# Kernel optimization log

Hardware: AMD Instinct MI355X
Metric: run time of the kernel (lower is better)

## Reference

```python
import math
import jax, jax.numpy as jnp
import numpy as np

DIM, HEADS, HD = 384, 12, 32
FEAT, WIN, SHIFT = (64, 64), (8, 8), (4, 4)
L = WIN[0] * WIN[1]  # window area = 64
MAX_LOGIT = math.log(1.0 / 0.01)


def _rel_log_coords():
    # pair-wise relative positions, log-spaced (static, numpy)
    coords = np.stack(np.meshgrid(np.arange(WIN[0]), np.arange(WIN[1]), indexing='ij'), 0).reshape(2, -1)
    rel = (coords[:, :, None] - coords[:, None, :]).transpose(1, 2, 0).reshape(-1, 2).astype(np.float32)
    return np.sign(rel) * np.log1p(np.abs(rel))  # [L*L, 2]


def _attn_mask():
    # shifted-window attention mask (static, numpy): 9 regions -> -100 across regions
    H, W = FEAT
    img = np.zeros((H, W), np.int32)
    cnt = 0
    for h0, h1 in ((0, H - WIN[0]), (H - WIN[0], H - SHIFT[0]), (H - SHIFT[0], H)):
        for w0, w1 in ((0, W - WIN[1]), (W - WIN[1], W - SHIFT[1]), (W - SHIFT[1], W)):
            img[h0:h1, w0:w1] = cnt
            cnt += 1
    mw = img.reshape(H // WIN[0], WIN[0], W // WIN[1], WIN[1]).transpose(0, 2, 1, 3).reshape(-1, L)
    diff = mw[:, None, :] - mw[:, :, None]
    return np.where(diff != 0, -100.0, 0.0).astype(np.float32)  # [nW, L, L]


def _ln(x, w, b, eps=1e-5):
    mu = x.mean(-1, keepdims=True)
    var = ((x - mu) ** 2).mean(-1, keepdims=True)
    return (x - mu) / jnp.sqrt(var + eps) * w + b


def setup_inputs() -> dict:
    key = jax.random.key(0)
    ks = jax.random.split(key, 12)
    B = 32
    s = 0.02
    return {
        'x': jax.random.normal(ks[0], (B, FEAT[0], FEAT[1], DIM), jnp.float32),
        'qkv_w': jax.random.normal(ks[1], (3 * DIM, DIM), jnp.float32) * s,
        'qkv_b': jnp.zeros((3 * DIM,), jnp.float32),
        'proj_w': jax.random.normal(ks[2], (DIM, DIM), jnp.float32) * s,
        'proj_b': jnp.zeros((DIM,), jnp.float32),
        'meta_w1': jax.random.normal(ks[3], (384, 2), jnp.float32) * 0.1,
        'meta_b1': jnp.zeros((384,), jnp.float32),
        'meta_w2': jax.random.normal(ks[4], (HEADS, 384), jnp.float32) * 0.1,
        'meta_b2': jnp.zeros((HEADS,), jnp.float32),
        'logit_scale': jnp.full((HEADS,), math.log(10.0), jnp.float32),
        'norm1_w': jnp.ones((DIM,), jnp.float32),
        'norm1_b': jnp.zeros((DIM,), jnp.float32),
        'fc1_w': jax.random.normal(ks[5], (4 * DIM, DIM), jnp.float32) * s,
        'fc1_b': jnp.zeros((4 * DIM,), jnp.float32),
        'fc2_w': jax.random.normal(ks[6], (DIM, 4 * DIM), jnp.float32) * s,
        'fc2_b': jnp.zeros((DIM,), jnp.float32),
        'norm2_w': jnp.ones((DIM,), jnp.float32),
        'norm2_b': jnp.zeros((DIM,), jnp.float32),
    }


def reference(x, qkv_w, qkv_b, proj_w, proj_b, meta_w1, meta_b1, meta_w2, meta_b2,
              logit_scale, norm1_w, norm1_b, fc1_w, fc1_b, fc2_w, fc2_b, norm2_w, norm2_b):
    B, H, W, C = x.shape
    wh, ww = WIN
    # cyclic shift + window partition: (B,H,W,C) -> (B*nW, L, C)
    sx = jnp.roll(x, (-SHIFT[0], -SHIFT[1]), axis=(1, 2))
    xw = sx.reshape(B, H // wh, wh, W // ww, ww, C).transpose(0, 1, 3, 2, 4, 5).reshape(-1, L, C)
    Bw = xw.shape[0]
    qkv = (xw @ qkv_w.T + qkv_b).reshape(Bw, L, 3, HEADS, HD).transpose(2, 0, 3, 1, 4)
    q, k, v = qkv[0], qkv[1], qkv[2]  # [Bw, heads, L, hd]
    # cosine attention
    qn = q / jnp.maximum(jnp.linalg.norm(q, axis=-1, keepdims=True), 1e-12)
    kn = k / jnp.maximum(jnp.linalg.norm(k, axis=-1, keepdims=True), 1e-12)
    attn = jnp.einsum('bhqd,bhkd->bhqk', qn, kn)
    scale = jnp.exp(jnp.minimum(logit_scale, MAX_LOGIT)).reshape(1, HEADS, 1, 1)
    # MLP-based relative position bias
    rel = jnp.asarray(_rel_log_coords())
    bias = jax.nn.relu(rel @ meta_w1.T + meta_b1) @ meta_w2.T + meta_b2  # [L*L, heads]
    bias = bias.T.reshape(HEADS, L, L)
    attn = attn * scale + bias[None]
    # shift mask
    mask = jnp.asarray(_attn_mask())  # [nW, L, L]
    nW = mask.shape[0]
    attn = attn.reshape(Bw // nW, nW, HEADS, L, L) + mask[None, :, None]
    attn = jax.nn.softmax(attn.reshape(Bw, HEADS, L, L), axis=-1)
    out = jnp.einsum('bhqk,bhkd->bhqd', attn, v).transpose(0, 2, 1, 3).reshape(Bw, L, C)
    out = out @ proj_w.T + proj_b
    # window reverse + reverse shift
    out = out.reshape(B, H // wh, W // ww, wh, ww, C).transpose(0, 1, 3, 2, 4, 5).reshape(B, H, W, C)
    out = jnp.roll(out, (SHIFT[0], SHIFT[1]), axis=(1, 2))
    # post-norm residuals (SwinV2Cr style)
    x = x + _ln(out, norm1_w, norm1_b)
    h = jax.nn.gelu(x @ fc1_w.T + fc1_b, approximate=False) @ fc2_w.T + fc2_b
    x = x + _ln(h, norm2_w, norm2_b)
    return x
```

## Files before the change

kernel.cpp:

```cpp
#include <hip/hip_runtime.h>
#include <hip/hip_bf16.h>

typedef __attribute__((ext_vector_type(4))) float f32x4;
typedef __attribute__((ext_vector_type(4))) unsigned int u32x4;
typedef __attribute__((ext_vector_type(8))) __bf16 bf16x8;

#define DEV static __device__ __forceinline__

DEV unsigned short f2bf(float f) {
  unsigned u = __builtin_bit_cast(unsigned, f);
  u += 0x7fffu + ((u >> 16) & 1u);
  return (unsigned short)(u >> 16);
}
DEV float bf2f(unsigned short b) {
  return __builtin_bit_cast(float, ((unsigned)b) << 16);
}
DEV unsigned pk2(float a, float b) {
  return (unsigned)f2bf(a) | ((unsigned)f2bf(b) << 16);
}
DEV unsigned cvtpk(float lo, float hi) {
  unsigned r;
  asm("v_cvt_pk_bf16_f32 %0, %1, %2" : "=v"(r) : "v"(lo), "v"(hi));
  return r;
}
DEV float fexp2(float x) {
  float r;
  asm("v_exp_f32 %0, %1" : "=v"(r) : "v"(x));
  return r;
}
DEV f32x4 mfma16(u32x4 a, u32x4 b, f32x4 c) {
  return __builtin_amdgcn_mfma_f32_16x16x32_bf16(
      __builtin_bit_cast(bf16x8, a), __builtin_bit_cast(bf16x8, b), c, 0, 0, 0);
}
DEV float ssq8(u32x4 c) {
  float s = 0.f;
#pragma unroll
  for (int e = 0; e < 4; e++) {
    float lo = __builtin_bit_cast(float, c[e] << 16);
    float hi = __builtin_bit_cast(float, c[e] & 0xffff0000u);
    s += lo * lo + hi * hi;
  }
  return s;
}
DEV void gload16(const unsigned short* g, unsigned short* l) {
  __builtin_amdgcn_global_load_lds(
      (const __attribute__((address_space(1))) unsigned int*)g,
      (__attribute__((address_space(3))) unsigned int*)l, 16, 0, 0);
}

template <int EPI>
__global__ __launch_bounds__(256) void gemm_lds(
    const unsigned short* __restrict__ A, const unsigned short* __restrict__ B,
    const float* __restrict__ bias, unsigned short* __restrict__ C,
    int N, int K, int nblocks) {
  __shared__ __align__(16) unsigned short As[3][128 * 32];
  __shared__ __align__(16) unsigned short Bs[3][128 * 32];
  const int bid = blockIdx.x;
  const int mchunk = (gridDim.x >> 3) / nblocks;
  const int xcd = bid & 7, idx = bid >> 3;
  const int nb = idx % nblocks, ml = idx / nblocks;
  const int m0 = (xcd * mchunk + ml) * 128, n0 = nb * 128;
  const int tid = threadIdx.x, w = tid >> 6, l = tid & 63;

  const int rs = l >> 2;
  const int gs = ((l & 3) ^ ((l >> 3) & 3)) * 8;
  const unsigned short* ag = A + (size_t)(m0 + w * 32 + rs) * K + gs;
  const unsigned short* bg = B + (size_t)(n0 + w * 32 + rs) * K + gs;
  const int seg = w * 1024;

  const int wm = (w >> 1) << 6, wn = (w & 1) << 6;
  const int lr = l & 15, lg = l >> 4;
  const int gsw = (lg ^ ((lr >> 1) & 3)) * 8;

  const f32x4 z4 = {0.f, 0.f, 0.f, 0.f};
  f32x4 acc[4][4];
#pragma unroll
  for (int i = 0; i < 4; i++)
#pragma unroll
    for (int j = 0; j < 4; j++) acc[i][j] = z4;

  auto stage = [&](int buf, int k0) {
    gload16(ag + k0, &As[buf][seg]);
    gload16(ag + (size_t)16 * K + k0, &As[buf][seg + 512]);
    gload16(bg + k0, &Bs[buf][seg]);
    gload16(bg + (size_t)16 * K + k0, &Bs[buf][seg + 512]);
  };
  auto compute = [&](int buf) {
    u32x4 a[4], b[4];
#pragma unroll
    for (int i = 0; i < 4; i++)
      a[i] = *(const u32x4*)(&As[buf][(wm + i * 16 + lr) * 32 + gsw]);
#pragma unroll
    for (int j = 0; j < 4; j++)
      b[j] = *(const u32x4*)(&Bs[buf][(wn + j * 16 + lr) * 32 + gsw]);
#pragma unroll
    for (int i = 0; i < 4; i++)
#pragma unroll
      for (int j = 0; j < 4; j++) acc[i][j] = mfma16(a[i], b[j], acc[i][j]);
  };

  const int nt = K >> 5;
  stage(0, 0);
  stage(1, 32);
  for (int t = 0; t < nt; ++t) {
    if (t + 1 < nt) {
      asm volatile("s_waitcnt vmcnt(4)" ::: "memory");
    } else {
      asm volatile("s_waitcnt vmcnt(0)" ::: "memory");
    }
    __builtin_amdgcn_s_barrier();
    __builtin_amdgcn_sched_barrier(0);
    if (t + 2 < nt) stage((t + 2) % 3, (t + 2) * 32);
    compute(t % 3);
  }

#pragma unroll
  for (int j = 0; j < 4; j++) {
    int ncol = n0 + wn + j * 16 + lr;
    float bv = bias[ncol];
#pragma unroll
    for (int i = 0; i < 4; i++) {
      int mbase = m0 + wm + i * 16 + lg * 4;
#pragma unroll
      for (int r = 0; r < 4; r++) {
        float v = acc[i][j][r] + bv;
        if (EPI == 1) v = 0.5f * v * (1.0f + erff(v * 0.70710678f));
        C[(size_t)(mbase + r) * N + ncol] = f2bf(v);
      }
    }
  }
}

template <int MODE>
__global__ __launch_bounds__(512) void gemm_ln(
    const unsigned short* __restrict__ A, const unsigned short* __restrict__ Bw,
    const float* __restrict__ bias, const float* __restrict__ resf,
    const unsigned short* __restrict__ resb, const float* __restrict__ nw,
    const float* __restrict__ nb, unsigned short* __restrict__ outb,
    float* __restrict__ outf, int K) {
  __shared__ __align__(16) unsigned short As[2][4096];
  __shared__ __align__(16) unsigned short Bs[2][12288];
  const int bid = blockIdx.x;
  const int swz = (bid & 7) * (gridDim.x >> 3) + (bid >> 3);
  const int m0 = swz * 128;
  const int tid = threadIdx.x, w8 = tid >> 6, l = tid & 63;
  const int lr = l & 15, lg = l >> 4;
  const int gsw = (lg ^ ((lr >> 1) & 3)) * 8;
  const int wm2 = (w8 >> 2) * 64;
  const int wn4 = w8 & 3;

  const int rs = l >> 2;
  const int gsrc = ((l & 3) ^ ((l >> 3) & 3)) * 8;
  const unsigned short* g_src[4];
  unsigned short* g_dst[4];
  int g_str[4];
#pragma unroll
  for (int i = 0; i < 4; i++) {
    int g = w8 * 4 + i;
    if (g < 8) {
      g_src[i] = A + (size_t)(m0 + g * 16 + rs) * K + gsrc;
      g_dst[i] = &As[0][g * 512];
      g_str[i] = 4096;
    } else {
      g_src[i] = Bw + (size_t)((g - 8) * 16 + rs) * K + gsrc;
      g_dst[i] = &Bs[0][(g - 8) * 512];
      g_str[i] = 12288;
    }
  }
  auto stage = [&](int buf, int k0) {
#pragma unroll
    for (int i = 0; i < 4; i++) gload16(g_src[i] + k0, g_dst[i] + buf * g_str[i]);
  };

  const f32x4 z4 = {0.f, 0.f, 0.f, 0.f};
  f32x4 acc[4][6];
#pragma unroll
  for (int i = 0; i < 4; i++)
#pragma unroll
    for (int j = 0; j < 6; j++) acc[i][j] = z4;

  auto compute = [&](int buf) {
    u32x4 a[4], b[6];
#pragma unroll
    for (int i = 0; i < 4; i++)
      a[i] = *(const u32x4*)(&As[buf][(wm2 + i * 16 + lr) * 32 + gsw]);
#pragma unroll
    for (int j = 0; j < 6; j++)
      b[j] = *(const u32x4*)(&Bs[buf][(wn4 * 96 + j * 16 + lr) * 32 + gsw]);
#pragma unroll
    for (int i = 0; i < 4; i++)
#pragma unroll
      for (int j = 0; j < 6; j++) acc[i][j] = mfma16(a[i], b[j], acc[i][j]);
  };

  const int nt = K >> 5;
  stage(0, 0);
  for (int t = 0; t < nt; ++t) {
    __syncthreads();
    if (t + 1 < nt) stage((t + 1) & 1, (t + 1) * 32);
    compute(t & 1);
  }

  float bcol[6];
#pragma unroll
  for (int j = 0; j < 6; j++) bcol[j] = bias[wn4 * 96 + j * 16 + lr];
#pragma unroll
  for (int i = 0; i < 4; i++)
#pragma unroll
    for (int j = 0; j < 6; j++)
#pragma unroll
      for (int r = 0; r < 4; r++) acc[i][j][r] += bcol[j];

  float* psum = (float*)(&As[0][0]);
  float* psq  = (float*)(&As[0][1024]);
#pragma unroll
  for (int i = 0; i < 4; i++)
#pragma unroll
    for (int r = 0; r < 4; r++) {
      float s1 = 0.f, s2 = 0.f;
#pragma unroll
      for (int j = 0; j < 6; j++) {
        float v = acc[i][j][r];
        s1 += v;
        s2 += v * v;
      }
#pragma unroll
      for (int d = 1; d < 16; d <<= 1) {
        s1 += __shfl_xor(s1, d, 64);
        s2 += __shfl_xor(s2, d, 64);
      }
      if (lr == 0) {
        int row = wm2 + i * 16 + lg * 4 + r;
        psum[wn4 * 128 + row] = s1;
        psq[wn4 * 128 + row] = s2;
      }
    }
  __syncthreads();

  float wcol[6], b2col[6];
#pragma unroll
  for (int j = 0; j < 6; j++) {
    int col = wn4 * 96 + j * 16 + lr;
    wcol[j] = nw[col];
    b2col[j] = nb[col];
  }
#pragma unroll
  for (int i = 0; i < 4; i++)
#pragma unroll
    for (int r = 0; r < 4; r++) {
      int row = wm2 + i * 16 + lg * 4 + r;
      float sum = psum[row] + psum[128 + row] + psum[256 + row] + psum[384 + row];
      float sq = psq[row] + psq[128 + row] + psq[256 + row] + psq[384 + row];
      float mu = sum * (1.f / 384.f);
      float rstd = rsqrtf(sq * (1.f / 384.f) - mu * mu + 1e-5f);
      size_t nbase;
      if (MODE == 0) {
        int mrow = m0 + row;
        int bb = mrow >> 12, widx = (mrow >> 6) & 63, tt = mrow & 63;
        int yy = (((widx >> 3) << 3) + (tt >> 3) + 4) & 63;
        int xx = (((widx & 7) << 3) + (tt & 7) + 4) & 63;
        nbase = (size_t)((bb << 12) | (yy << 6) | xx) * 384;
      } else {
        nbase = (size_t)(m0 + row) * 384;
      }
#pragma unroll
      for (int j = 0; j < 6; j++) {
        int col = wn4 * 96 + j * 16 + lr;
        float v = (acc[i][j][r] - mu) * rstd * wcol[j] + b2col[j];
        if (MODE == 0) {
          outb[nbase + col] = f2bf(resf[nbase + col] + v);
        } else {
          outf[nbase + col] = bf2f(resb[nbase + col]) + v;
        }
      }
    }
}

__global__ __launch_bounds__(256) void gather_cvt(
    const float* __restrict__ x, unsigned short* __restrict__ xb) {
  int wv = threadIdx.x >> 6, l = threadIdx.x & 63;
  int m = blockIdx.x * 4 + wv;
  int w = m >> 6, t = m & 63;
  int b = w >> 6, wy = (w >> 3) & 7, wx = w & 7;
  int oy = (wy * 8 + (t >> 3) + 4) & 63;
  int ox = (wx * 8 + (t & 7) + 4) & 63;
  const float2* src =
      (const float2*)(x + (size_t)((((b << 6) | oy) << 6) | ox) * 384 + l * 6);
  float2 f0 = src[0], f1 = src[1], f2 = src[2];
  unsigned* dst = (unsigned*)(xb + (size_t)m * 384 + l * 6);
  dst[0] = pk2(f0.x, f0.y);
  dst[1] = pk2(f1.x, f1.y);
  dst[2] = pk2(f2.x, f2.y);
}

__global__ __launch_bounds__(256, 4) void attn_win(
    const unsigned short* __restrict__ qkv, const float* __restrict__ btab2,
    const float* __restrict__ lscale, unsigned short* __restrict__ aout) {
  __shared__ __align__(16) unsigned short vT[4][32 * 72];
  __shared__ __align__(16) float rnk[4][64];
  const int w = blockIdx.x;
  const int wv = threadIdx.x >> 6, l = threadIdx.x & 63;
  const int h = blockIdx.y * 4 + wv;
  const int lr = l & 15, lg = l >> 4;
  const size_t base = (size_t)w * 64 * 1152 + h * 32;
  const f32x4 z4 = {0.f, 0.f, 0.f, 0.f};

  {
    const u32x4* vp = (const u32x4*)(qkv + base + (size_t)l * 1152 + 768);
#pragma unroll
    for (int c4 = 0; c4 < 4; c4++) {
      u32x4 c = vp[c4];
#pragma unroll
      for (int e = 0; e < 4; e++) {
        vT[wv][(c4 * 8 + e * 2) * 72 + l] = (unsigned short)(c[e] & 0xffffu);
        vT[wv][(c4 * 8 + e * 2 + 1) * 72 + l] = (unsigned short)(c[e] >> 16);
      }
    }
  }
  u32x4 kf[4];
#pragma unroll
  for (int tj = 0; tj < 4; tj++) {
    kf[tj] = *(const u32x4*)(qkv + base + (size_t)(tj * 16 + lr) * 1152 + 384 + lg * 8);
    float s = ssq8(kf[tj]);
    s += __shfl_xor(s, 16, 64);
    s += __shfl_xor(s, 32, 64);
    if (lg == 0) rnk[wv][tj * 16 + lr] = rsqrtf(fmaxf(s, 1e-24f));
  }
  u32x4 qf[4];
  float rnq[4];
#pragma unroll
  for (int ti = 0; ti < 4; ti++) {
    qf[ti] = *(const u32x4*)(qkv + base + (size_t)(ti * 16 + lr) * 1152 + lg * 8);
    float s = ssq8(qf[ti]);
    s += __shfl_xor(s, 16, 64);
    s += __shfl_xor(s, 32, 64);
    rnq[ti] = rsqrtf(fmaxf(s, 1e-24f));
  }
  __syncthreads();

  u32x4 vb[2][2];
#pragma unroll
  for (int kc = 0; kc < 2; kc++)
#pragma unroll
    for (int tj2 = 0; tj2 < 2; tj2++)
      vb[kc][tj2] = *(const u32x4*)(&vT[wv][(tj2 * 16 + lr) * 72 + kc * 32 + lg * 8]);

  const float scl2 = expf(fminf(lscale[h], 4.6051702f)) * 1.44269504f;
  const int wt = ((((w >> 3) & 7) == 7) ? 2 : 0) | (((w & 7) == 7) ? 1 : 0);
  const float* tabh = btab2 + (((size_t)wt * 12 + h) << 12);
  const int s0l = lr + ((l & 16) ? 32 : 0);
  const int s1l = s0l + 16;
  const bool hi = (l & 32) != 0;

#pragma unroll
  for (int ti = 0; ti < 4; ti++) {
    f32x4 sv[4];
#pragma unroll
    for (int tj = 0; tj < 4; tj++) sv[tj] = mfma16(kf[tj], qf[ti], z4);
    const float* tab = tabh + ((ti * 16 + lr) << 6);
    const float cb = rnq[ti] * scl2;
    f32x4 val[4];
    float m = -1e30f;
#pragma unroll
    for (int tj = 0; tj < 4; tj++) {
      f32x4 rk4 = *(const f32x4*)(&rnk[wv][tj * 16 + lg * 4]);
      f32x4 t4 = *(const f32x4*)(tab + tj * 16 + lg * 4);
#pragma unroll
      for (int r = 0; r < 4; r++) {
        float v = sv[tj][r] * (cb * rk4[r]) + t4[r];
        val[tj][r] = v;
        m = fmaxf(m, v);
      }
    }
    m = fmaxf(m, __shfl_xor(m, 16, 64));
    m = fmaxf(m, __shfl_xor(m, 32, 64));
    float den = 0.f;
#pragma unroll
    for (int tj = 0; tj < 4; tj++)
#pragma unroll
      for (int r = 0; r < 4; r++) {
        float p = fexp2(val[tj][r] - m);
        val[tj][r] = p;
        den += p;
      }
    den += __shfl_xor(den, 16, 64);
    den += __shfl_xor(den, 32, 64);
    float rden = 1.f / den;
#pragma unroll
    for (int tj = 0; tj < 4; tj++)
#pragma unroll
      for (int r = 0; r < 4; r++) val[tj][r] *= rden;

    f32x4 o[2] = {z4, z4};
#pragma unroll
    for (int kc = 0; kc < 2; kc++) {
      unsigned yA0 = cvtpk(val[2 * kc][0], val[2 * kc][1]);
      unsigned yA1 = cvtpk(val[2 * kc][2], val[2 * kc][3]);
      unsigned yB0 = cvtpk(val[2 * kc + 1][0], val[2 * kc + 1][1]);
      unsigned yB1 = cvtpk(val[2 * kc + 1][2], val[2 * kc + 1][3]);
      unsigned a0 = __shfl((int)yA0, s0l, 64), b0 = __shfl((int)yB0, s0l, 64);
      unsigned a1 = __shfl((int)yA1, s0l, 64), b1 = __shfl((int)yB1, s0l, 64);
      unsigned a2 = __shfl((int)yA0, s1l, 64), b2 = __shfl((int)yB0, s1l, 64);
      unsigned a3 = __shfl((int)yA1, s1l, 64), b3 = __shfl((int)yB1, s1l, 64);
      u32x4 pa = {hi ? b0 : a0, hi ? b1 : a1, hi ? b2 : a2, hi ? b3 : a3};
#pragma unroll
      for (int tj2 = 0; tj2 < 2; tj2++) o[tj2] = mfma16(pa, vb[kc][tj2], o[tj2]);
    }
#pragma unroll
    for (int tj2 = 0; tj2 < 2; tj2++)
#pragma unroll
      for (int r = 0; r < 4; r++)
        aout[(size_t)(w * 64 + ti * 16 + lg * 4 + r) * 384 + h * 32 + tj2 * 16 + lr] =
            f2bf(o[tj2][r]);
  }
}

__global__ __launch_bounds__(256) void btab2_kernel(
    const float* __restrict__ w1, const float* __restrict__ b1,
    const float* __restrict__ w2, const float* __restrict__ b2,
    float* __restrict__ btab2) {
  int p = blockIdx.x * 256 + threadIdx.x;
  int i = p >> 6, j = p & 63;
  float dy = (float)((i >> 3) - (j >> 3));
  float dx = (float)((i & 7) - (j & 7));
  float r0 = (dy > 0.f ? 1.f : (dy < 0.f ? -1.f : 0.f)) * log1pf(fabsf(dy));
  float r1 = (dx > 0.f ? 1.f : (dx < 0.f ? -1.f : 0.f)) * log1pf(fabsf(dx));
  float acc[12];
#pragma unroll
  for (int hh = 0; hh < 12; hh++) acc[hh] = b2[hh];
  for (int c = 0; c < 384; c++) {
    float hv = w1[c * 2] * r0 + w1[c * 2 + 1] * r1 + b1[c];
    hv = fmaxf(hv, 0.f);
#pragma unroll
    for (int hh = 0; hh < 12; hh++) acc[hh] += hv * w2[hh * 384 + c];
  }
  bool ddy = ((i >> 3) >= 4) != ((j >> 3) >= 4);
  bool ddx = ((i & 7) >= 4) != ((j & 7) >= 4);
  const float L2E = 1.44269504f;
#pragma unroll
  for (int wt = 0; wt < 4; wt++) {
    float mask = ((((wt >> 1) != 0) && ddy) || (((wt & 1) != 0) && ddx)) ? -100.f : 0.f;
#pragma unroll
    for (int hh = 0; hh < 12; hh++)
      btab2[(((size_t)wt * 12 + hh) << 12) + p] = (acc[hh] + mask) * L2E;
  }
}

__global__ __launch_bounds__(256) void cvt_kernel(
    const float* __restrict__ s, unsigned short* __restrict__ d, int n) {
  int i = blockIdx.x * 256 + threadIdx.x;
  if (i < n) d[i] = f2bf(s[i]);
}

extern "C" void kernel_launch(void* const* d_in, const int* in_sizes, int n_in,
                              void* d_out, int out_size, void* d_ws,
                              size_t ws_size, hipStream_t stream) {
  (void)in_sizes; (void)n_in; (void)out_size; (void)ws_size;
  const float* x      = (const float*)d_in[0];
  const float* qkv_w  = (const float*)d_in[1];
  const float* qkv_b  = (const float*)d_in[2];
  const float* proj_w = (const float*)d_in[3];
  const float* proj_b = (const float*)d_in[4];
  const float* mw1    = (const float*)d_in[5];
  const float* mb1    = (const float*)d_in[6];
  const float* mw2    = (const float*)d_in[7];
  const float* mb2    = (const float*)d_in[8];
  const float* lsc    = (const float*)d_in[9];
  const float* n1w    = (const float*)d_in[10];
  const float* n1b    = (const float*)d_in[11];
  const float* w1     = (const float*)d_in[12];
  const float* b1     = (const float*)d_in[13];
  const float* w2     = (const float*)d_in[14];
  const float* b2     = (const float*)d_in[15];
  const float* n2w    = (const float*)d_in[16];
  const float* n2b    = (const float*)d_in[17];

  char* ws = (char*)d_ws;
  unsigned short* wqb  = (unsigned short*)(ws + 0);
  unsigned short* wpb  = (unsigned short*)(ws + 884736);
  unsigned short* w1b  = (unsigned short*)(ws + 1179648);
  unsigned short* w2b  = (unsigned short*)(ws + 2359296);
  float* btab2         = (float*)(ws + 3538944);
  unsigned short* xb   = (unsigned short*)(ws + 4718592);
  unsigned short* qkvb = (unsigned short*)(ws + 105381888);
  unsigned short* att  = (unsigned short*)(ws + 407371776);
  unsigned short* hb   = (unsigned short*)(ws + 508035072);
  unsigned short* y1b  = xb;
  float* yout = (float*)d_out;

  cvt_kernel<<<dim3(1728), 256, 0, stream>>>(qkv_w, wqb, 442368);
  cvt_kernel<<<dim3(576), 256, 0, stream>>>(proj_w, wpb, 147456);
  cvt_kernel<<<dim3(2304), 256, 0, stream>>>(w1, w1b, 589824);
  cvt_kernel<<<dim3(2304), 256, 0, stream>>>(w2, w2b, 589824);
  btab2_kernel<<<dim3(16), 256, 0, stream>>>(mw1, mb1, mw2, mb2, btab2);
  gather_cvt<<<dim3(32768), 256, 0, stream>>>(x, xb);

  gemm_lds<0><<<dim3(9216), 256, 0, stream>>>(xb, wqb, qkv_b, qkvb, 1152, 384, 9);
  attn_win<<<dim3(2048, 3), 256, 0, stream>>>(qkvb, btab2, lsc, att);
  gemm_ln<0><<<dim3(1024), 512, 0, stream>>>(
      att, wpb, proj_b, x, nullptr, n1w, n1b, y1b, nullptr, 384);
  for (int c = 0; c < 4; c++) {
    const unsigned short* ya = y1b + (size_t)c * 32768 * 384;
    float* yc = yout + (size_t)c * 32768 * 384;
    gemm_lds<1><<<dim3(3072), 256, 0, stream>>>(ya, w1b, b1, hb, 1536, 384, 12);
    gemm_ln<1><<<dim3(256), 512, 0, stream>>>(
        hb, w2b, b2, nullptr, ya, n2w, n2b, nullptr, yc, 1536);
  }
}
```

Measured before the change: 1.284 ms.

## Replace 128x128 GEMM with 256x256-tile 8-wave kernel and pad QKV to 1280

Replaces the 128x128-tile, 4-wave bf16 GEMM used for the QKV and FC1 projections with a 256x256-tile, 8-wave kernel. It uses a BK of 64, a two-stage LDS double buffer with XOR swizzle, interleaved global-to-LDS prefetch between MFMA phases, and s_setprio around the MFMA blocks. Because the output width 1152 does not divide by 256, the QKV weight and bias are zero-padded to 1280 rows and the attention kernel reads with the padded stride. The aim is more reuse per LDS byte and fewer redundant global loads, at the cost of about 11% extra QKV compute and writes, higher register pressure, and a larger intermediate buffer.

```diff
diff --git a/kernel.cpp b/kernel.cpp
--- a/kernel.cpp
+++ b/kernel.cpp
@@ -49,85 +49,155 @@
 }
 
 template <int EPI>
-__global__ __launch_bounds__(256) void gemm_lds(
+__global__ __launch_bounds__(512, 2) void gemm8(
     const unsigned short* __restrict__ A, const unsigned short* __restrict__ B,
     const float* __restrict__ bias, unsigned short* __restrict__ C,
-    int N, int K, int nblocks) {
-  __shared__ __align__(16) unsigned short As[3][128 * 32];
-  __shared__ __align__(16) unsigned short Bs[3][128 * 32];
+    int Nld, int K, int nblocks) {
+  __shared__ __align__(16) unsigned short As[2][256 * 64];
+  __shared__ __align__(16) unsigned short Bs[2][256 * 64];
   const int bid = blockIdx.x;
   const int mchunk = (gridDim.x >> 3) / nblocks;
   const int xcd = bid & 7, idx = bid >> 3;
   const int nb = idx % nblocks, ml = idx / nblocks;
-  const int m0 = (xcd * mchunk + ml) * 128, n0 = nb * 128;
+  const int m0 = (xcd * mchunk + ml) * 256, n0 = nb * 256;
   const int tid = threadIdx.x, w = tid >> 6, l = tid & 63;
-
-  const int rs = l >> 2;
-  const int gs = ((l & 3) ^ ((l >> 3) & 3)) * 8;
-  const unsigned short* ag = A + (size_t)(m0 + w * 32 + rs) * K + gs;
-  const unsigned short* bg = B + (size_t)(n0 + w * 32 + rs) * K + gs;
-  const int seg = w * 1024;
-
-  const int wm = (w >> 1) << 6, wn = (w & 1) << 6;
   const int lr = l & 15, lg = l >> 4;
-  const int gsw = (lg ^ ((lr >> 1) & 3)) * 8;
+  const int wm = (w >> 2) * 128, wn = (w & 3) * 64;
+  const int srow = l >> 3;
+  const int scol = ((l & 7) ^ srow) * 8;
+  const int NT = K >> 6;
+
+  auto stA = [&](int p, int kt, int half, int j) {
+    int r = half * 128 + w * 16 + j * 8;
+    gload16(A + (size_t)(m0 + r + srow) * K + kt * 64 + scol, &As[p][r * 64]);
+  };
+  auto stB = [&](int p, int kt, int half, int j) {
+    int r = half * 128 + w * 16 + j * 8;
+    gload16(B + (size_t)(n0 + r + srow) * K + kt * 64 + scol, &Bs[p][r * 64]);
+  };
 
   const f32x4 z4 = {0.f, 0.f, 0.f, 0.f};
-  f32x4 acc[4][4];
-#pragma unroll
-  for (int i = 0; i < 4; i++)
+  f32x4 acc[8][4];
+#pragma unroll
+  for (int i = 0; i < 8; i++)
 #pragma unroll
     for (int j = 0; j < 4; j++) acc[i][j] = z4;
-
-  auto stage = [&](int buf, int k0) {
-    gload16(ag + k0, &As[buf][seg]);
-    gload16(ag + (size_t)16 * K + k0, &As[buf][seg + 512]);
-    gload16(bg + k0, &Bs[buf][seg]);
-    gload16(bg + (size_t)16 * K + k0, &Bs[buf][seg + 512]);
-  };
-  auto compute = [&](int buf) {
-    u32x4 a[4], b[4];
-#pragma unroll
-    for (int i = 0; i < 4; i++)
-      a[i] = *(const u32x4*)(&As[buf][(wm + i * 16 + lr) * 32 + gsw]);
-#pragma unroll
-    for (int j = 0; j < 4; j++)
-      b[j] = *(const u32x4*)(&Bs[buf][(wn + j * 16 + lr) * 32 + gsw]);
-#pragma unroll
-    for (int i = 0; i < 4; i++)
-#pragma unroll
-      for (int j = 0; j < 4; j++) acc[i][j] = mfma16(a[i], b[j], acc[i][j]);
-  };
-
-  const int nt = K >> 5;
-  stage(0, 0);
-  stage(1, 32);
-  for (int t = 0; t < nt; ++t) {
-    if (t + 1 < nt) {
-      asm volatile("s_waitcnt vmcnt(4)" ::: "memory");
+  u32x4 af[8], bf[8];
+
+#pragma unroll
+  for (int ktp = 0; ktp < 2; ktp++) {
+    stB(ktp, ktp, 0, 0); stB(ktp, ktp, 0, 1);
+    stB(ktp, ktp, 1, 0); stB(ktp, ktp, 1, 1);
+    stA(ktp, ktp, 0, 0); stA(ktp, ktp, 0, 1);
+    stA(ktp, ktp, 1, 0); stA(ktp, ktp, 1, 1);
+  }
+
+  for (int kt = 0; kt < NT; ++kt) {
+    const int p = kt & 1;
+    if (kt + 1 < NT) {
+      asm volatile("s_waitcnt vmcnt(8)" ::: "memory");
     } else {
       asm volatile("s_waitcnt vmcnt(0)" ::: "memory");
     }
     __builtin_amdgcn_s_barrier();
+
+#pragma unroll
+    for (int ni = 0; ni < 4; ni++)
+#pragma unroll
+      for (int ks = 0; ks < 2; ks++) {
+        int R = wn + ni * 16 + lr;
+        bf[ni * 2 + ks] =
+            *(const u32x4*)&Bs[p][R * 64 + (((ks * 4 + lg) ^ (lr & 7)) * 8)];
+      }
+#pragma unroll
+    for (int mi = 0; mi < 4; mi++)
+#pragma unroll
+      for (int ks = 0; ks < 2; ks++) {
+        int R = wm + mi * 16 + lr;
+        af[mi * 2 + ks] =
+            *(const u32x4*)&As[p][R * 64 + (((ks * 4 + lg) ^ (lr & 7)) * 8)];
+      }
+    asm volatile("s_waitcnt lgkmcnt(0)" ::: "memory");
     __builtin_amdgcn_sched_barrier(0);
-    if (t + 2 < nt) stage((t + 2) % 3, (t + 2) * 32);
-    compute(t % 3);
-  }
-
-#pragma unroll
-  for (int j = 0; j < 4; j++) {
-    int ncol = n0 + wn + j * 16 + lr;
+    __builtin_amdgcn_s_setprio(1);
+#pragma unroll
+    for (int mi = 0; mi < 4; mi++)
+#pragma unroll
+      for (int ni = 0; ni < 2; ni++)
+#pragma unroll
+        for (int ks = 0; ks < 2; ks++)
+          acc[mi][ni] = mfma16(af[mi * 2 + ks], bf[ni * 2 + ks], acc[mi][ni]);
+    __builtin_amdgcn_s_setprio(0);
+    __builtin_amdgcn_s_barrier();
+
+    if (kt + 2 < NT) { stB(p, kt + 2, 0, 0); stB(p, kt + 2, 0, 1); }
+    __builtin_amdgcn_s_setprio(1);
+#pragma unroll
+    for (int mi = 0; mi < 4; mi++)
+#pragma unroll
+      for (int ni = 0; ni < 2; ni++)
+#pragma unroll
+        for (int ks = 0; ks < 2; ks++)
+          acc[mi][ni + 2] =
+              mfma16(af[mi * 2 + ks], bf[(ni + 2) * 2 + ks], acc[mi][ni + 2]);
+    __builtin_amdgcn_s_setprio(0);
+    __builtin_amdgcn_s_barrier();
+
+#pragma unroll
+    for (int mi = 0; mi < 4; mi++)
+#pragma unroll
+      for (int ks = 0; ks < 2; ks++) {
+        int R = wm + 64 + mi * 16 + lr;
+        af[mi * 2 + ks] =
+            *(const u32x4*)&As[p][R * 64 + (((ks * 4 + lg) ^ (lr & 7)) * 8)];
+      }
+    if (kt + 2 < NT) { stB(p, kt + 2, 1, 0); stB(p, kt + 2, 1, 1); }
+    asm volatile("s_waitcnt lgkmcnt(0)" ::: "memory");
+    __builtin_amdgcn_sched_barrier(0);
+    __builtin_amdgcn_s_setprio(1);
+#pragma unroll
+    for (int mi = 0; mi < 4; mi++)
+#pragma unroll
+      for (int ni = 0; ni < 2; ni++)
+#pragma unroll
+        for (int ks = 0; ks < 2; ks++)
+          acc[mi + 4][ni] =
+              mfma16(af[mi * 2 + ks], bf[ni * 2 + ks], acc[mi + 4][ni]);
+    __builtin_amdgcn_s_setprio(0);
+    __builtin_amdgcn_s_barrier();
+
+    if (kt + 2 < NT) {
+      stA(p, kt + 2, 0, 0); stA(p, kt + 2, 0, 1);
+      stA(p, kt + 2, 1, 0); stA(p, kt + 2, 1, 1);
+    }
+    __builtin_amdgcn_s_setprio(1);
+#pragma unroll
+    for (int mi = 0; mi < 4; mi++)
+#pragma unroll
+      for (int ni = 0; ni < 2; ni++)
+#pragma unroll
+        for (int ks = 0; ks < 2; ks++)
+          acc[mi + 4][ni + 2] =
+              mfma16(af[mi * 2 + ks], bf[(ni + 2) * 2 + ks], acc[mi + 4][ni + 2]);
+    __builtin_amdgcn_s_setprio(0);
+  }
+
+#pragma unroll
+  for (int ni = 0; ni < 4; ni++) {
+    int ncol = n0 + wn + ni * 16 + lr;
     float bv = bias[ncol];
 #pragma unroll
-    for (int i = 0; i < 4; i++) {
-      int mbase = m0 + wm + i * 16 + lg * 4;
-#pragma unroll
-      for (int r = 0; r < 4; r++) {
-        float v = acc[i][j][r] + bv;
-        if (EPI == 1) v = 0.5f * v * (1.0f + erff(v * 0.70710678f));
-        C[(size_t)(mbase + r) * N + ncol] = f2bf(v);
-      }
-    }
+    for (int mh = 0; mh < 2; mh++)
+#pragma unroll
+      for (int mi = 0; mi < 4; mi++) {
+        int mbase = m0 + wm + mh * 64 + mi * 16 + lg * 4;
+#pragma unroll
+        for (int r = 0; r < 4; r++) {
+          float v = acc[mh * 4 + mi][ni][r] + bv;
+          if (EPI == 1) v = 0.5f * v * (1.0f + erff(v * 0.70710678f));
+          C[(size_t)(mbase + r) * Nld + ncol] = f2bf(v);
+        }
+      }
   }
 }
 
@@ -302,11 +372,11 @@
   const int wv = threadIdx.x >> 6, l = threadIdx.x & 63;
   const int h = blockIdx.y * 4 + wv;
   const int lr = l & 15, lg = l >> 4;
-  const size_t base = (size_t)w * 64 * 1152 + h * 32;
+  const size_t base = (size_t)w * 64 * 1280 + h * 32;
   const f32x4 z4 = {0.f, 0.f, 0.f, 0.f};
 
   {
-    const u32x4* vp = (const u32x4*)(qkv + base + (size_t)l * 1152 + 768);
+    const u32x4* vp = (const u32x4*)(qkv + base + (size_t)l * 1280 + 768);
 #pragma unroll
     for (int c4 = 0; c4 < 4; c4++) {
       u32x4 c = vp[c4];
@@ -320,7 +390,7 @@
   u32x4 kf[4];
 #pragma unroll
   for (int tj = 0; tj < 4; tj++) {
-    kf[tj] = *(const u32x4*)(qkv + base + (size_t)(tj * 16 + lr) * 1152 + 384 + lg * 8);
+    kf[tj] = *(const u32x4*)(qkv + base + (size_t)(tj * 16 + lr) * 1280 + 384 + lg * 8);
     float s = ssq8(kf[tj]);
     s += __shfl_xor(s, 16, 64);
     s += __shfl_xor(s, 32, 64);
@@ -330,7 +400,7 @@
   float rnq[4];
 #pragma unroll
   for (int ti = 0; ti < 4; ti++) {
-    qf[ti] = *(const u32x4*)(qkv + base + (size_t)(ti * 16 + lr) * 1152 + lg * 8);
+    qf[ti] = *(const u32x4*)(qkv + base + (size_t)(ti * 16 + lr) * 1280 + lg * 8);
     float s = ssq8(qf[ti]);
     s += __shfl_xor(s, 16, 64);
     s += __shfl_xor(s, 32, 64);
@@ -450,6 +520,19 @@
     const float* __restrict__ s, unsigned short* __restrict__ d, int n) {
   int i = blockIdx.x * 256 + threadIdx.x;
   if (i < n) d[i] = f2bf(s[i]);
+}
+
+__global__ __launch_bounds__(256) void cvt_pad_kernel(
+    const float* __restrict__ s, unsigned short* __restrict__ d, int n_src,
+    int n_tot) {
+  int i = blockIdx.x * 256 + threadIdx.x;
+  if (i < n_tot) d[i] = (i < n_src) ? f2bf(s[i]) : (unsigned short)0;
+}
+
+__global__ __launch_bounds__(256) void pad_bias_kernel(
+    const float* __restrict__ s, float* __restrict__ d) {
+  int i = blockIdx.x * 256 + threadIdx.x;
+  if (i < 1280) d[i] = (i < 1152) ? s[i] : 0.f;
 }
 
 extern "C" void kernel_launch(void* const* d_in, const int* in_sizes, int n_in,
@@ -477,32 +560,34 @@
 
   char* ws = (char*)d_ws;
   unsigned short* wqb  = (unsigned short*)(ws + 0);
-  unsigned short* wpb  = (unsigned short*)(ws + 884736);
-  unsigned short* w1b  = (unsigned short*)(ws + 1179648);
-  unsigned short* w2b  = (unsigned short*)(ws + 2359296);
-  float* btab2         = (float*)(ws + 3538944);
+  unsigned short* wpb  = (unsigned short*)(ws + 1048576);
+  unsigned short* w1b  = (unsigned short*)(ws + 1441792);
+  unsigned short* w2b  = (unsigned short*)(ws + 2621440);
+  float* qbp           = (float*)(ws + 3801088);
+  float* btab2         = (float*)(ws + 3866624);
   unsigned short* xb   = (unsigned short*)(ws + 4718592);
   unsigned short* qkvb = (unsigned short*)(ws + 105381888);
-  unsigned short* att  = (unsigned short*)(ws + 407371776);
-  unsigned short* hb   = (unsigned short*)(ws + 508035072);
+  unsigned short* att  = (unsigned short*)(ws + 440926208);
+  unsigned short* hb   = (unsigned short*)(ws + 541589504);
   unsigned short* y1b  = xb;
   float* yout = (float*)d_out;
 
-  cvt_kernel<<<dim3(1728), 256, 0, stream>>>(qkv_w, wqb, 442368);
+  cvt_pad_kernel<<<dim3(1920), 256, 0, stream>>>(qkv_w, wqb, 442368, 491520);
   cvt_kernel<<<dim3(576), 256, 0, stream>>>(proj_w, wpb, 147456);
   cvt_kernel<<<dim3(2304), 256, 0, stream>>>(w1, w1b, 589824);
   cvt_kernel<<<dim3(2304), 256, 0, stream>>>(w2, w2b, 589824);
+  pad_bias_kernel<<<dim3(5), 256, 0, stream>>>(qkv_b, qbp);
   btab2_kernel<<<dim3(16), 256, 0, stream>>>(mw1, mb1, mw2, mb2, btab2);
   gather_cvt<<<dim3(32768), 256, 0, stream>>>(x, xb);
 
-  gemm_lds<0><<<dim3(9216), 256, 0, stream>>>(xb, wqb, qkv_b, qkvb, 1152, 384, 9);
+  gemm8<0><<<dim3(2560), 512, 0, stream>>>(xb, wqb, qbp, qkvb, 1280, 384, 5);
   attn_win<<<dim3(2048, 3), 256, 0, stream>>>(qkvb, btab2, lsc, att);
   gemm_ln<0><<<dim3(1024), 512, 0, stream>>>(
       att, wpb, proj_b, x, nullptr, n1w, n1b, y1b, nullptr, 384);
   for (int c = 0; c < 4; c++) {
     const unsigned short* ya = y1b + (size_t)c * 32768 * 384;
     float* yc = yout + (size_t)c * 32768 * 384;
-    gemm_lds<1><<<dim3(3072), 256, 0, stream>>>(ya, w1b, b1, hb, 1536, 384, 12);
+    gemm8<1><<<dim3(768), 512, 0, stream>>>(ya, w1b, b1, hb, 1536, 384, 6);
     gemm_ln<1><<<dim3(256), 512, 0, stream>>>(
         hb, w2b, b2, nullptr, ya, n2w, n2b, nullptr, yc, 1536);
   }
```

New measurement: 1.287 ms. No clear change (+0.2%).
